# Performance work log

Hardware: AMD Instinct MI355X
Metric: run time of the kernel (lower is better)

Reference implementation:

```python
import jax, jax.numpy as jnp
import numpy as np

HIDDEN = 768
NUM_HEADS = 12
HEAD_DIM = HIDDEN // NUM_HEADS
B, S = 4, 2048


def setup_inputs() -> dict:
    key = jax.random.key(0)
    ks = jax.random.split(key, 10)
    scale = 1.0 / np.sqrt(HIDDEN)
    return {
        "hidden_states": jax.random.normal(ks[0], (B, S, HIDDEN), dtype=jnp.float32),
        "attention_mask": jnp.ones((B, S), dtype=jnp.float32),
        "Wq": jax.random.normal(ks[1], (HIDDEN, HIDDEN), dtype=jnp.float32) * scale,
        "bq": jnp.zeros((HIDDEN,), dtype=jnp.float32),
        "Wk": jax.random.normal(ks[2], (HIDDEN, HIDDEN), dtype=jnp.float32) * scale,
        "bk": jnp.zeros((HIDDEN,), dtype=jnp.float32),
        "Wv": jax.random.normal(ks[3], (HIDDEN, HIDDEN), dtype=jnp.float32) * scale,
        "bv": jnp.zeros((HIDDEN,), dtype=jnp.float32),
        "Wo": jax.random.normal(ks[4], (HIDDEN, HIDDEN), dtype=jnp.float32) * scale,
        "bo": jnp.zeros((HIDDEN,), dtype=jnp.float32),
    }


def reference(hidden_states, attention_mask, Wq, bq, Wk, bk, Wv, bv, Wo, bo):
    b, s, _ = hidden_states.shape
    # nn.Linear: x @ W.T + b  (W is [out, in])
    Q = hidden_states @ Wq.T + bq
    K = hidden_states @ Wk.T + bk
    V = hidden_states @ Wv.T + bv
    # [b, s, h*d] -> [b, h, s, d]
    Q = Q.reshape(b, s, NUM_HEADS, HEAD_DIM).transpose(0, 2, 1, 3)
    K = K.reshape(b, s, NUM_HEADS, HEAD_DIM).transpose(0, 2, 1, 3)
    V = V.reshape(b, s, NUM_HEADS, HEAD_DIM).transpose(0, 2, 1, 3)
    # scores: [b, h, s, s]
    scores = jnp.einsum("bhqd,bhkd->bhqk", Q, K) / jnp.sqrt(
        jnp.asarray(HEAD_DIM, dtype=Q.dtype))
    # mask: [b, s] -> additive bias broadcast over heads and query dim
    bias = (1.0 - attention_mask)[:, None, None, :] * -10000.0
    scores = scores + bias
    probs = jax.nn.softmax(scores, axis=-1)  # dropout p=0.0 -> identity
    context = jnp.einsum("bhqk,bhkd->bhqd", probs, V)
    context = context.transpose(0, 2, 1, 3).reshape(b, s, HIDDEN)
    return context @ Wo.T + bo
```

## Files before the change

kernel.cpp:

```cpp
#include <hip/hip_runtime.h>
#include <hip/hip_bf16.h>

#define SEQ   2048
#define NH    12
#define MTOK  8192

typedef __attribute__((ext_vector_type(8))) short short8;
typedef __attribute__((ext_vector_type(4))) short short4v;
typedef __attribute__((ext_vector_type(4))) float f32x4;

__device__ inline short f2bf(float x) {
  __hip_bfloat16 h = __float2bfloat16(x);
  return *(short*)&h;
}

#define GLL(gp, lp) __builtin_amdgcn_global_load_lds( \
    (const __attribute__((address_space(1))) void*)(gp), \
    (__attribute__((address_space(3))) void*)(lp), 16, 0, 0)

#define MFMA(a, b, c) __builtin_amdgcn_mfma_f32_16x16x32_bf16(a, b, c, 0, 0, 0)

#if !defined(__HIP_DEVICE_COMPILE__)
#define MFMA16(a, b, c) (c)
#elif __has_builtin(__builtin_amdgcn_mfma_f32_16x16x16bf16_1k)
#define MFMA16(a, b, c) __builtin_amdgcn_mfma_f32_16x16x16bf16_1k(a, b, c, 0, 0, 0)
#elif __has_builtin(__builtin_amdgcn_mfma_f32_16x16x16_bf16)
#define MFMA16(a, b, c) __builtin_amdgcn_mfma_f32_16x16x16_bf16(a, b, c, 0, 0, 0)
#else
#error "no 16x16x16 bf16 mfma builtin on device"
#endif

#if !defined(__HIP_DEVICE_COMPILE__)
#define EXP2(x) (x)
#elif __has_builtin(__builtin_amdgcn_exp2f)
#define EXP2(x) __builtin_amdgcn_exp2f(x)
#else
#define EXP2(x) __expf((x) * 0.6931471805599453f)
#endif

__device__ inline unsigned pack2bf(float a, float b) {
  unsigned ua = __float_as_uint(a) + 0x8000u;
  unsigned ub = __float_as_uint(b) + 0x8000u;
#if defined(__HIP_DEVICE_COMPILE__) && __has_builtin(__builtin_amdgcn_perm)
  return __builtin_amdgcn_perm(ub, ua, 0x07060302u);
#else
  return (ub & 0xFFFF0000u) | (ua >> 16);
#endif
}

union PackFrag {
  unsigned u[2];
  short4v s;
};

#define QSCALE 0.18033688011112042f
#define MBSCALE -14426.950408889634f

__global__ __launch_bounds__(256) void to_bf16(
    const float* __restrict__ in, short* __restrict__ out, int n4) {
  int i = blockIdx.x * 256 + threadIdx.x;
  if (i >= n4) return;
  float4 v = ((const float4*)in)[i];
  short4v o;
  o[0] = f2bf(v.x); o[1] = f2bf(v.y); o[2] = f2bf(v.z); o[3] = f2bf(v.w);
  ((short4v*)out)[i] = o;
}

__global__ __launch_bounds__(256) void conv_wqkv(
    const float* __restrict__ Wq, const float* __restrict__ Wk,
    const float* __restrict__ Wv, short* __restrict__ out) {
  int idx = blockIdx.x * 256 + threadIdx.x;
  int r = idx / 192, c = (idx - r * 192) * 4;
  const float* src = r < 768 ? &Wq[(size_t)r * 768]
                   : r < 1536 ? &Wk[(size_t)(r - 768) * 768]
                              : &Wv[(size_t)(r - 1536) * 768];
  float4 v = *(const float4*)&src[c];
  short4v o;
  o[0] = f2bf(v.x); o[1] = f2bf(v.y); o[2] = f2bf(v.z); o[3] = f2bf(v.w);
  *(short4v*)&out[(size_t)r * 768 + c] = o;
}

__global__ __launch_bounds__(256) void maskbias(
    const float* __restrict__ mask, float* __restrict__ mb) {
  int i = blockIdx.x * 256 + threadIdx.x;
  if (i < MTOK) mb[i] = (1.f - mask[i]) * MBSCALE;
}

__global__ __launch_bounds__(256) void gemm_qkv(
    const short* __restrict__ A, const short* __restrict__ B,
    const float* __restrict__ bq, const float* __restrict__ bk,
    const float* __restrict__ bv, short* __restrict__ Qb,
    short* __restrict__ Kb, short* __restrict__ Vt) {
  __shared__ __align__(16) short As[128 * 32];
  __shared__ __align__(16) short Bs[128 * 32];
  const int t = threadIdx.x;
  const int wid = t >> 6, lane = t & 63, l15 = lane & 15, quad = lane >> 4;
  const int bm = blockIdx.x * 128, bn = blockIdx.y * 128;
  const int mq = (wid & 1) * 64, nq = (wid >> 1) * 64;
  const int srow = lane >> 2, scol = (lane & 3) * 8;

  f32x4 acc[4][4] = {};
  const short* gA0 = A + (size_t)(bm + wid * 16 + srow) * 768 + scol;
  const short* gA1 = A + (size_t)(bm + 64 + wid * 16 + srow) * 768 + scol;
  const short* gB0 = B + (size_t)(bn + wid * 16 + srow) * 768 + scol;
  const short* gB1 = B + (size_t)(bn + 64 + wid * 16 + srow) * 768 + scol;

  for (int k0 = 0; k0 < 768; k0 += 32) {
    GLL(gA0 + k0, &As[(wid * 16) * 32]);
    GLL(gA1 + k0, &As[(64 + wid * 16) * 32]);
    GLL(gB0 + k0, &Bs[(wid * 16) * 32]);
    GLL(gB1 + k0, &Bs[(64 + wid * 16) * 32]);
    __syncthreads();
    short8 a[4], b[4];
#pragma unroll
    for (int mt = 0; mt < 4; ++mt)
      a[mt] = *(const short8*)&As[(mq + mt * 16 + l15) * 32 + quad * 8];
#pragma unroll
    for (int nt = 0; nt < 4; ++nt)
      b[nt] = *(const short8*)&Bs[(nq + nt * 16 + l15) * 32 + quad * 8];
#pragma unroll
    for (int mt = 0; mt < 4; ++mt)
#pragma unroll
      for (int nt = 0; nt < 4; ++nt)
        acc[mt][nt] = MFMA(a[mt], b[nt], acc[mt][nt]);
    __syncthreads();
  }

  const int seg = bn >= 1536 ? 2 : (bn >= 768 ? 1 : 0);
  const float* bias = seg == 0 ? bq : (seg == 1 ? bk : bv);
  const int colbase = bn - seg * 768;

  if (seg < 2) {
    short* dst = seg == 0 ? Qb : Kb;
    const float sc = seg == 0 ? QSCALE : 1.f;
#pragma unroll
    for (int mt = 0; mt < 4; ++mt)
#pragma unroll
      for (int nt = 0; nt < 4; ++nt) {
        int col = colbase + nq + nt * 16 + l15;
        float bias_v = bias[col];
#pragma unroll
        for (int i = 0; i < 4; ++i) {
          int row = bm + mq + mt * 16 + quad * 4 + i;
          dst[(size_t)row * 768 + col] = f2bf((acc[mt][nt][i] + bias_v) * sc);
        }
      }
  } else {
#pragma unroll
    for (int mt = 0; mt < 4; ++mt) {
      int row0 = bm + mq + mt * 16 + quad * 4;
      int b_ = row0 >> 11, s = row0 & 2047;
#pragma unroll
      for (int nt = 0; nt < 4; ++nt) {
        int col = colbase + nq + nt * 16 + l15;
        float bias_v = bias[col];
        int h = col >> 6, d = col & 63;
        short4v pv;
#pragma unroll
        for (int i = 0; i < 4; ++i) pv[i] = f2bf(acc[mt][nt][i] + bias_v);
        *(short4v*)&Vt[(((size_t)b_ * NH + h) * 64 + d) * 2048 + s] = pv;
      }
    }
  }
}

__global__ __launch_bounds__(256, 3) void attn_v7(
    const short* __restrict__ Qb, const short* __restrict__ Kb,
    const short* __restrict__ Vt, const float* __restrict__ maskb,
    short* __restrict__ Ctx) {
  __shared__ __align__(16) short Ks[64 * 64];
  __shared__ __align__(16) short Vs[64 * 64];
  const int t = threadIdx.x;
  const int w = t >> 6, lane = t & 63, l15 = lane & 15, quad = lane >> 4;
  const int bh = blockIdx.x, b = bh / NH, h = bh % NH;
  const int q0 = blockIdx.y * 128;

  short8 qa[2][2];
#pragma unroll
  for (int qt = 0; qt < 2; ++qt)
#pragma unroll
    for (int ks = 0; ks < 2; ++ks) {
      int row = b * 2048 + q0 + w * 32 + qt * 16 + l15;
      qa[qt][ks] = *(const short8*)&Qb[(size_t)row * 768 + h * 64 + ks * 32 + quad * 8];
    }

  f32x4 O[2][4] = {};
  f32x4 lacc[2] = {};
  short4v ones4;
#pragma unroll
  for (int j = 0; j < 4; ++j) ones4[j] = (short)0x3F80;

  const int r0 = w * 16 + (lane >> 3);
  const int pc = lane & 7;
  const int swz0 = (pc ^ (r0 & 7)) * 8;
  const int swz1 = (pc ^ ((r0 + 8) & 7)) * 8;
  const short* gK0 = Kb + (size_t)(b * 2048 + r0) * 768 + h * 64 + swz0;
  const short* gK1 = Kb + (size_t)(b * 2048 + r0 + 8) * 768 + h * 64 + swz1;
  const short* gV0 = Vt + ((size_t)bh * 64 + r0) * 2048 + swz0;
  const short* gV1 = Vt + ((size_t)bh * 64 + r0 + 8) * 2048 + swz1;
  const float* mb = maskb + b * 2048;
  const int rs = l15 & 7;

  for (int k0 = 0; k0 < SEQ; k0 += 64) {
    GLL(gK0 + (size_t)k0 * 768, &Ks[(w * 16) * 64]);
    GLL(gK1 + (size_t)k0 * 768, &Ks[(w * 16 + 8) * 64]);
    GLL(gV0 + k0, &Vs[(w * 16) * 64]);
    GLL(gV1 + k0, &Vs[(w * 16 + 8) * 64]);
    __syncthreads();

    f32x4 S[4][2] = {};
#pragma unroll
    for (int ks = 0; ks < 2; ++ks) {
      short8 kb[4];
#pragma unroll
      for (int kt = 0; kt < 4; ++kt)
        kb[kt] = *(const short8*)&Ks[(kt * 16 + l15) * 64 +
                                     (((ks * 4 + quad) ^ rs) * 8)];
#pragma unroll
      for (int kt = 0; kt < 4; ++kt) {
        S[kt][0] = MFMA(kb[kt], qa[0][ks], S[kt][0]);
        S[kt][1] = MFMA(kb[kt], qa[1][ks], S[kt][1]);
      }
    }

    short4v pb[4][2];
#pragma unroll
    for (int kt = 0; kt < 4; ++kt) {
      float4 mb4 = *(const float4*)&mb[k0 + kt * 16 + quad * 4];
#pragma unroll
      for (int qt = 0; qt < 2; ++qt) {
        float p0 = EXP2(S[kt][qt][0] + mb4.x);
        float p1 = EXP2(S[kt][qt][1] + mb4.y);
        float p2 = EXP2(S[kt][qt][2] + mb4.z);
        float p3 = EXP2(S[kt][qt][3] + mb4.w);
        PackFrag pf;
        pf.u[0] = pack2bf(p0, p1);
        pf.u[1] = pack2bf(p2, p3);
        pb[kt][qt] = pf.s;
      }
    }

#pragma unroll
    for (int kt = 0; kt < 4; ++kt) {
      lacc[0] = MFMA16(ones4, pb[kt][0], lacc[0]);
      lacc[1] = MFMA16(ones4, pb[kt][1], lacc[1]);
    }

#pragma unroll
    for (int kt = 0; kt < 4; ++kt) {
#pragma unroll
      for (int dt = 0; dt < 4; ++dt) {
        short4v av = *(const short4v*)&Vs[(dt * 16 + l15) * 64 +
            (((kt * 2 + (quad >> 1)) ^ rs) * 8) + (quad & 1) * 4];
        O[0][dt] = MFMA16(av, pb[kt][0], O[0][dt]);
        O[1][dt] = MFMA16(av, pb[kt][1], O[1][dt]);
      }
    }
    __syncthreads();
  }

#pragma unroll
  for (int qt = 0; qt < 2; ++qt) {
    float inv = 1.f / lacc[qt][0];
    int row = b * 2048 + q0 + w * 32 + qt * 16 + l15;
#pragma unroll
    for (int dt = 0; dt < 4; ++dt) {
      PackFrag pf;
      pf.u[0] = pack2bf(O[qt][dt][0] * inv, O[qt][dt][1] * inv);
      pf.u[1] = pack2bf(O[qt][dt][2] * inv, O[qt][dt][3] * inv);
      *(short4v*)&Ctx[(size_t)row * 768 + h * 64 + dt * 16 + quad * 4] = pf.s;
    }
  }
}

__global__ __launch_bounds__(256) void gemm_out(
    const short* __restrict__ A, const short* __restrict__ B,
    const float* __restrict__ bias, float* __restrict__ C) {
  __shared__ __align__(16) short As[128 * 32];
  __shared__ __align__(16) short Bs[128 * 32];
  const int t = threadIdx.x;
  const int wid = t >> 6, lane = t & 63, l15 = lane & 15, quad = lane >> 4;
  const int bm = blockIdx.x * 128, bn = blockIdx.y * 128;
  const int mq = (wid & 1) * 64, nq = (wid >> 1) * 64;
  const int srow = lane >> 2, scol = (lane & 3) * 8;

  f32x4 acc[4][4] = {};
  const short* gA0 = A + (size_t)(bm + wid * 16 + srow) * 768 + scol;
  const short* gA1 = A + (size_t)(bm + 64 + wid * 16 + srow) * 768 + scol;
  const short* gB0 = B + (size_t)(bn + wid * 16 + srow) * 768 + scol;
  const short* gB1 = B + (size_t)(bn + 64 + wid * 16 + srow) * 768 + scol;

  for (int k0 = 0; k0 < 768; k0 += 32) {
    GLL(gA0 + k0, &As[(wid * 16) * 32]);
    GLL(gA1 + k0, &As[(64 + wid * 16) * 32]);
    GLL(gB0 + k0, &Bs[(wid * 16) * 32]);
    GLL(gB1 + k0, &Bs[(64 + wid * 16) * 32]);
    __syncthreads();
    short8 a[4], b[4];
#pragma unroll
    for (int mt = 0; mt < 4; ++mt)
      a[mt] = *(const short8*)&As[(mq + mt * 16 + l15) * 32 + quad * 8];
#pragma unroll
    for (int nt = 0; nt < 4; ++nt)
      b[nt] = *(const short8*)&Bs[(nq + nt * 16 + l15) * 32 + quad * 8];
#pragma unroll
    for (int mt = 0; mt < 4; ++mt)
#pragma unroll
      for (int nt = 0; nt < 4; ++nt)
        acc[mt][nt] = MFMA(a[mt], b[nt], acc[mt][nt]);
    __syncthreads();
  }

#pragma unroll
  for (int mt = 0; mt < 4; ++mt)
#pragma unroll
    for (int nt = 0; nt < 4; ++nt) {
      int col = bn + nq + nt * 16 + l15;
      float bias_v = bias[col];
#pragma unroll
      for (int i = 0; i < 4; ++i) {
        int row = bm + mq + mt * 16 + quad * 4 + i;
        C[(size_t)row * 768 + col] = acc[mt][nt][i] + bias_v;
      }
    }
}

extern "C" void kernel_launch(void* const* d_in, const int* in_sizes, int n_in,
                              void* d_out, int out_size, void* d_ws,
                              size_t ws_size, hipStream_t stream) {
  const float* hs   = (const float*)d_in[0];
  const float* mask = (const float*)d_in[1];
  const float* Wq   = (const float*)d_in[2];
  const float* bq   = (const float*)d_in[3];
  const float* Wk   = (const float*)d_in[4];
  const float* bk   = (const float*)d_in[5];
  const float* Wv   = (const float*)d_in[6];
  const float* bv   = (const float*)d_in[7];
  const float* Wo   = (const float*)d_in[8];
  const float* bo   = (const float*)d_in[9];

  char* ws = (char*)d_ws;
  short* Xb    = (short*)(ws);
  short* Wqkvb = (short*)(ws + 12582912);
  short* Wob   = (short*)(ws + 16121856);
  short* Qb    = (short*)(ws + 17301504);
  short* Kb    = (short*)(ws + 29884416);
  short* Vtg   = (short*)(ws + 42467328);
  short* Ctxb  = (short*)(ws + 55050240);
  float* mbias = (float*)(ws + 67633152);

  to_bf16<<<6144, 256, 0, stream>>>(hs, Xb, 1572864);
  conv_wqkv<<<1728, 256, 0, stream>>>(Wq, Wk, Wv, Wqkvb);
  to_bf16<<<576, 256, 0, stream>>>(Wo, Wob, 147456);
  maskbias<<<32, 256, 0, stream>>>(mask, mbias);

  gemm_qkv<<<dim3(64, 18), 256, 0, stream>>>(Xb, Wqkvb, bq, bk, bv,
                                             Qb, Kb, Vtg);
  attn_v7<<<dim3(48, 16), 256, 0, stream>>>(Qb, Kb, Vtg, mbias, Ctxb);
  gemm_out<<<dim3(64, 6), 256, 0, stream>>>(Ctxb, Wob, bo, (float*)d_out);
}
```

Before: 237.4 us.

## Use BK=64 tiles with XOR-swizzled LDS in both GEMMs and merge weight conversions

Both projection GEMMs now stage 64-wide K slices instead of 32, which halves the number of barrier pairs per tile. The LDS layout gets an XOR swizzle on the 16-byte chunk index to avoid bank conflicts on the fragment reads. The Wo conversion is folded into the combined weight-conversion kernel, removing one launch. Shared memory per block doubles, which can lower occupancy.

Result: no change. 236.0 us (-0.6%).

```diff
diff --git a/kernel.cpp b/kernel.cpp
--- a/kernel.cpp
+++ b/kernel.cpp
@@ -66,18 +66,23 @@
   ((short4v*)out)[i] = o;
 }
 
-__global__ __launch_bounds__(256) void conv_wqkv(
+__global__ __launch_bounds__(256) void conv_w(
     const float* __restrict__ Wq, const float* __restrict__ Wk,
-    const float* __restrict__ Wv, short* __restrict__ out) {
+    const float* __restrict__ Wv, const float* __restrict__ Wo,
+    short* __restrict__ Wqkvb, short* __restrict__ Wob) {
   int idx = blockIdx.x * 256 + threadIdx.x;
   int r = idx / 192, c = (idx - r * 192) * 4;
-  const float* src = r < 768 ? &Wq[(size_t)r * 768]
-                   : r < 1536 ? &Wk[(size_t)(r - 768) * 768]
-                              : &Wv[(size_t)(r - 1536) * 768];
-  float4 v = *(const float4*)&src[c];
+  const float* src;
+  short* dst;
+  int rr;
+  if (r < 768)       { src = Wq; rr = r;        dst = Wqkvb; }
+  else if (r < 1536) { src = Wk; rr = r - 768;  dst = Wqkvb; }
+  else if (r < 2304) { src = Wv; rr = r - 1536; dst = Wqkvb; }
+  else               { src = Wo; rr = r - 2304; dst = Wob; r = rr; }
+  float4 v = *(const float4*)&src[(size_t)rr * 768 + c];
   short4v o;
   o[0] = f2bf(v.x); o[1] = f2bf(v.y); o[2] = f2bf(v.z); o[3] = f2bf(v.w);
-  *(short4v*)&out[(size_t)r * 768 + c] = o;
+  *(short4v*)&dst[(size_t)r * 768 + c] = o;
 }
 
 __global__ __launch_bounds__(256) void maskbias(
@@ -85,46 +90,51 @@
   int i = blockIdx.x * 256 + threadIdx.x;
   if (i < MTOK) mb[i] = (1.f - mask[i]) * MBSCALE;
 }
+
+#define GEMM_BK64_LOOP(Aptr, Bptr)                                            \
+  __shared__ __align__(16) short As[128 * 64];                                \
+  __shared__ __align__(16) short Bs[128 * 64];                                \
+  const int t = threadIdx.x;                                                  \
+  const int wid = t >> 6, lane = t & 63, l15 = lane & 15, quad = lane >> 4;   \
+  const int bm = blockIdx.x * 128, bn = blockIdx.y * 128;                     \
+  const int mq = (wid & 1) * 64, nq = (wid >> 1) * 64;                        \
+  const int srow8 = lane >> 3;           \
+  const int schunk = lane & 7;                        \
+  const int scol = (schunk ^ srow8) * 8;    \
+  f32x4 acc[4][4] = {};                                                       \
+  const short *gA[4], *gB[4];                                                 \
+  _Pragma("unroll") for (int g = 0; g < 4; ++g) {                             \
+    int row = wid * 32 + g * 8 + srow8;                                       \
+    gA[g] = (Aptr) + (size_t)(bm + row) * 768 + scol;                         \
+    gB[g] = (Bptr) + (size_t)(bn + row) * 768 + scol;                         \
+  }                                                                           \
+  for (int k0 = 0; k0 < 768; k0 += 64) {                                      \
+    _Pragma("unroll") for (int g = 0; g < 4; ++g)                             \
+      GLL(gA[g] + k0, &As[(wid * 32 + g * 8) * 64]);                          \
+    _Pragma("unroll") for (int g = 0; g < 4; ++g)                             \
+      GLL(gB[g] + k0, &Bs[(wid * 32 + g * 8) * 64]);                          \
+    __syncthreads();                                                          \
+    _Pragma("unroll") for (int ks = 0; ks < 2; ++ks) {                        \
+      short8 a[4], b[4];                                                      \
+      _Pragma("unroll") for (int mt = 0; mt < 4; ++mt)                        \
+        a[mt] = *(const short8*)&As[(mq + mt * 16 + l15) * 64 +               \
+                                    (((ks * 4 + quad) ^ (l15 & 7)) * 8)];     \
+      _Pragma("unroll") for (int nt = 0; nt < 4; ++nt)                        \
+        b[nt] = *(const short8*)&Bs[(nq + nt * 16 + l15) * 64 +               \
+                                    (((ks * 4 + quad) ^ (l15 & 7)) * 8)];     \
+      _Pragma("unroll") for (int mt = 0; mt < 4; ++mt)                        \
+        _Pragma("unroll") for (int nt = 0; nt < 4; ++nt)                      \
+          acc[mt][nt] = MFMA(a[mt], b[nt], acc[mt][nt]);                      \
+    }                                                                         \
+    __syncthreads();                                                          \
+  }
 
 __global__ __launch_bounds__(256) void gemm_qkv(
     const short* __restrict__ A, const short* __restrict__ B,
     const float* __restrict__ bq, const float* __restrict__ bk,
     const float* __restrict__ bv, short* __restrict__ Qb,
     short* __restrict__ Kb, short* __restrict__ Vt) {
-  __shared__ __align__(16) short As[128 * 32];
-  __shared__ __align__(16) short Bs[128 * 32];
-  const int t = threadIdx.x;
-  const int wid = t >> 6, lane = t & 63, l15 = lane & 15, quad = lane >> 4;
-  const int bm = blockIdx.x * 128, bn = blockIdx.y * 128;
-  const int mq = (wid & 1) * 64, nq = (wid >> 1) * 64;
-  const int srow = lane >> 2, scol = (lane & 3) * 8;
-
-  f32x4 acc[4][4] = {};
-  const short* gA0 = A + (size_t)(bm + wid * 16 + srow) * 768 + scol;
-  const short* gA1 = A + (size_t)(bm + 64 + wid * 16 + srow) * 768 + scol;
-  const short* gB0 = B + (size_t)(bn + wid * 16 + srow) * 768 + scol;
-  const short* gB1 = B + (size_t)(bn + 64 + wid * 16 + srow) * 768 + scol;
-
-  for (int k0 = 0; k0 < 768; k0 += 32) {
-    GLL(gA0 + k0, &As[(wid * 16) * 32]);
-    GLL(gA1 + k0, &As[(64 + wid * 16) * 32]);
-    GLL(gB0 + k0, &Bs[(wid * 16) * 32]);
-    GLL(gB1 + k0, &Bs[(64 + wid * 16) * 32]);
-    __syncthreads();
-    short8 a[4], b[4];
-#pragma unroll
-    for (int mt = 0; mt < 4; ++mt)
-      a[mt] = *(const short8*)&As[(mq + mt * 16 + l15) * 32 + quad * 8];
-#pragma unroll
-    for (int nt = 0; nt < 4; ++nt)
-      b[nt] = *(const short8*)&Bs[(nq + nt * 16 + l15) * 32 + quad * 8];
-#pragma unroll
-    for (int mt = 0; mt < 4; ++mt)
-#pragma unroll
-      for (int nt = 0; nt < 4; ++nt)
-        acc[mt][nt] = MFMA(a[mt], b[nt], acc[mt][nt]);
-    __syncthreads();
-  }
+  GEMM_BK64_LOOP(A, B)
 
   const int seg = bn >= 1536 ? 2 : (bn >= 768 ? 1 : 0);
   const float* bias = seg == 0 ? bq : (seg == 1 ? bk : bv);
@@ -162,6 +172,25 @@
       }
     }
   }
+}
+
+__global__ __launch_bounds__(256) void gemm_out(
+    const short* __restrict__ A, const short* __restrict__ B,
+    const float* __restrict__ bias, float* __restrict__ C) {
+  GEMM_BK64_LOOP(A, B)
+
+#pragma unroll
+  for (int mt = 0; mt < 4; ++mt)
+#pragma unroll
+    for (int nt = 0; nt < 4; ++nt) {
+      int col = bn + nq + nt * 16 + l15;
+      float bias_v = bias[col];
+#pragma unroll
+      for (int i = 0; i < 4; ++i) {
+        int row = bm + mq + mt * 16 + quad * 4 + i;
+        C[(size_t)row * 768 + col] = acc[mt][nt][i] + bias_v;
+      }
+    }
 }
 
 __global__ __launch_bounds__(256, 3) void attn_v7(
@@ -271,58 +300,6 @@
       *(short4v*)&Ctx[(size_t)row * 768 + h * 64 + dt * 16 + quad * 4] = pf.s;
     }
   }
-}
-
-__global__ __launch_bounds__(256) void gemm_out(
-    const short* __restrict__ A, const short* __restrict__ B,
-    const float* __restrict__ bias, float* __restrict__ C) {
-  __shared__ __align__(16) short As[128 * 32];
-  __shared__ __align__(16) short Bs[128 * 32];
-  const int t = threadIdx.x;
-  const int wid = t >> 6, lane = t & 63, l15 = lane & 15, quad = lane >> 4;
-  const int bm = blockIdx.x * 128, bn = blockIdx.y * 128;
-  const int mq = (wid & 1) * 64, nq = (wid >> 1) * 64;
-  const int srow = lane >> 2, scol = (lane & 3) * 8;
-
-  f32x4 acc[4][4] = {};
-  const short* gA0 = A + (size_t)(bm + wid * 16 + srow) * 768 + scol;
-  const short* gA1 = A + (size_t)(bm + 64 + wid * 16 + srow) * 768 + scol;
-  const short* gB0 = B + (size_t)(bn + wid * 16 + srow) * 768 + scol;
-  const short* gB1 = B + (size_t)(bn + 64 + wid * 16 + srow) * 768 + scol;
-
-  for (int k0 = 0; k0 < 768; k0 += 32) {
-    GLL(gA0 + k0, &As[(wid * 16) * 32]);
-    GLL(gA1 + k0, &As[(64 + wid * 16) * 32]);
-    GLL(gB0 + k0, &Bs[(wid * 16) * 32]);
-    GLL(gB1 + k0, &Bs[(64 + wid * 16) * 32]);
-    __syncthreads();
-    short8 a[4], b[4];
-#pragma unroll
-    for (int mt = 0; mt < 4; ++mt)
-      a[mt] = *(const short8*)&As[(mq + mt * 16 + l15) * 32 + quad * 8];
-#pragma unroll
-    for (int nt = 0; nt < 4; ++nt)
-      b[nt] = *(const short8*)&Bs[(nq + nt * 16 + l15) * 32 + quad * 8];
-#pragma unroll
-    for (int mt = 0; mt < 4; ++mt)
-#pragma unroll
-      for (int nt = 0; nt < 4; ++nt)
-        acc[mt][nt] = MFMA(a[mt], b[nt], acc[mt][nt]);
-    __syncthreads();
-  }
-
-#pragma unroll
-  for (int mt = 0; mt < 4; ++mt)
-#pragma unroll
-    for (int nt = 0; nt < 4; ++nt) {
-      int col = bn + nq + nt * 16 + l15;
-      float bias_v = bias[col];
-#pragma unroll
-      for (int i = 0; i < 4; ++i) {
-        int row = bm + mq + mt * 16 + quad * 4 + i;
-        C[(size_t)row * 768 + col] = acc[mt][nt][i] + bias_v;
-      }
-    }
 }
 
 extern "C" void kernel_launch(void* const* d_in, const int* in_sizes, int n_in,
@@ -350,8 +327,7 @@
   float* mbias = (float*)(ws + 67633152);
 
   to_bf16<<<6144, 256, 0, stream>>>(hs, Xb, 1572864);
-  conv_wqkv<<<1728, 256, 0, stream>>>(Wq, Wk, Wv, Wqkvb);
-  to_bf16<<<576, 256, 0, stream>>>(Wo, Wob, 147456);
+  conv_w<<<2304, 256, 0, stream>>>(Wq, Wk, Wv, Wo, Wqkvb, Wob);
   maskbias<<<32, 256, 0, stream>>>(mask, mbias);
 
   gemm_qkv<<<dim3(64, 18), 256, 0, stream>>>(Xb, Wqkvb, bq, bk, bv,
```
